# Performance work log

Measured on AMD Instinct MI355X. Metric: run time of the kernel, lower is better.

## Reference

```python
import jax, jax.numpy as jnp
from jax import lax
import numpy as np

B = 8
NUM_ANCHORS = 1047552
PROPOSAL_COUNT = 1000
NMS_THRESHOLD = 0.7
RPN_BBOX_STD_DEV = np.array([0.1, 0.1, 0.2, 0.2], dtype=np.float32)
RPN_NMS_LIMIT = 6000


def setup_inputs() -> dict:
    key = jax.random.key(0)
    k1, k2, k3 = jax.random.split(key, 3)
    rpn_scores = jax.random.uniform(k1, (B, NUM_ANCHORS, 2), dtype=jnp.float32)
    rpn_bbox_delta = jax.random.normal(k2, (B, NUM_ANCHORS, 4), dtype=jnp.float32)
    # Build valid normalized anchors (y1,x1,y2,x2) from uniform randoms.
    u = jax.random.uniform(k3, (NUM_ANCHORS, 4), dtype=jnp.float32)
    cy, cx = u[:, 0], u[:, 1]
    h = u[:, 2] * 0.2 + 0.01
    w = u[:, 3] * 0.2 + 0.01
    anchors = jnp.stack([cy - 0.5 * h, cx - 0.5 * w, cy + 0.5 * h, cx + 0.5 * w], axis=-1)
    anchors = jnp.clip(anchors, 0.0, 1.0)
    return {"rpn_scores": rpn_scores, "rpn_bbox_delta": rpn_bbox_delta, "anchors": anchors}


def _apply_box_deltas(boxes, deltas):
    # boxes: [..., (y1,x1,y2,x2)], deltas: [..., (dy,dx,log(dh),log(dw))]
    h = boxes[..., 2] - boxes[..., 0]
    w = boxes[..., 3] - boxes[..., 1]
    cy = boxes[..., 0] + 0.5 * h + deltas[..., 0] * h
    cx = boxes[..., 1] + 0.5 * w + deltas[..., 1] * w
    h = h * jnp.exp(deltas[..., 2])
    w = w * jnp.exp(deltas[..., 3])
    y1 = cy - 0.5 * h
    x1 = cx - 0.5 * w
    return jnp.stack([y1, x1, y1 + h, x1 + w], axis=-1)


def _nms_indices(boxes):
    # Greedy NMS over boxes already sorted by descending score. boxes: [N,4].
    N = boxes.shape[0]
    areas = (boxes[:, 2] - boxes[:, 0]) * (boxes[:, 3] - boxes[:, 1])

    def body(i, state):
        valid, sel = state
        idx = jnp.argmax(valid)          # first still-valid box = highest score
        has = valid[idx]
        sel = sel.at[i].set(jnp.where(has, idx, -1))
        b = boxes[idx]
        yy1 = jnp.maximum(b[0], boxes[:, 0])
        xx1 = jnp.maximum(b[1], boxes[:, 1])
        yy2 = jnp.minimum(b[2], boxes[:, 2])
        xx2 = jnp.minimum(b[3], boxes[:, 3])
        inter = jnp.maximum(yy2 - yy1, 0.0) * jnp.maximum(xx2 - xx1, 0.0)
        union = areas[idx] + areas - inter
        iou = jnp.where(union > 0, inter / union, 0.0)
        keep = valid & (iou <= NMS_THRESHOLD)
        keep = keep.at[idx].set(False)
        valid = jnp.where(has, keep, valid)
        return valid, sel

    valid0 = jnp.ones((N,), dtype=bool)
    sel0 = jnp.full((PROPOSAL_COUNT,), -1, dtype=jnp.int32)
    _, sel = lax.fori_loop(0, PROPOSAL_COUNT, body, (valid0, sel0))
    return sel


def _nms_single(boxes):
    # boxes: [pre_nms_limit, 4] sorted by score desc -> [proposal_count, 4], zero-padded
    sel = _nms_indices(lax.stop_gradient(boxes))
    props = boxes[jnp.clip(sel, 0)]
    return jnp.where(sel[:, None] >= 0, props, 0.0)


def _forward(rpn_scores, rpn_bbox_delta, anchors):
    scores = rpn_scores[:, :, 1]                                   # [B, A]
    deltas = rpn_bbox_delta * jnp.asarray(RPN_BBOX_STD_DEV)        # [B, A, 4]
    pre_nms_limit = min(RPN_NMS_LIMIT, anchors.shape[0])
    top_scores, ix = lax.top_k(scores, pre_nms_limit)              # [B, pre]
    tgt_deltas = jnp.take_along_axis(deltas, ix[..., None], axis=1)  # [B, pre, 4]
    tgt_anchors = anchors[ix]                                      # [B, pre, 4]
    boxes = _apply_box_deltas(tgt_anchors, tgt_deltas)
    boxes = jnp.clip(boxes, 0.0, 1.0)                              # window (0,0,1,1)
    proposals = jax.vmap(_nms_single)(boxes)                       # [B, proposal_count, 4]
    return proposals


def reference(rpn_scores, rpn_bbox_delta, anchors):
    return _forward(rpn_scores, rpn_bbox_delta, anchors)
```

## Files before the change

kernel.cpp:

```cpp
#include <hip/hip_runtime.h>
#include <stdint.h>

#define NBATCH   8
#define NA       1047552
#define PRE_NMS  6000
#define NPROP    1000
#define BINS     2048
#define HB       64
#define GB       128
#define CAND_CAP 8192
#define NMS_THR  0.7f
#define GBUF     1024
#define SCAP     2048
#define PCHUNK   32
#define PCAP     256
#define REJW     188

#define OFF_HIST  ((size_t)0)
#define OFF_BOFF  (OFF_HIST + (size_t)NBATCH*HB*BINS*2)
#define OFF_BCNT  (OFF_BOFF + (size_t)NBATCH*BINS*4)
#define OFF_CTR   (OFF_BCNT + (size_t)NBATCH*BINS*4)
#define CTR_BYTES ((size_t)(32 + NBATCH*PCHUNK*4 + NBATCH*BINS*4))
#define OFF_CAND  (OFF_CTR + 66624)
#define OFF_BOXES (OFF_CAND + (size_t)NBATCH*CAND_CAP*8)
#define OFF_PAIRS (OFF_BOXES + (size_t)NBATCH*PRE_NMS*16)
#define WS_NEEDED (OFF_PAIRS + (size_t)NBATCH*PCHUNK*PCAP*4)

__device__ __forceinline__ unsigned score_bin(float s) {
    int b = (int)(s * (float)BINS);
    if (b < 0) b = 0;
    if (b > BINS - 1) b = BINS - 1;
    return (unsigned)b;
}

__global__ __launch_bounds__(256) void k_hist(const float* __restrict__ scores,
                                              uint16_t* __restrict__ hist) {
    __shared__ uint32_t lh[BINS];
    const int b = blockIdx.y;
    for (int t = threadIdx.x; t < BINS; t += 256) lh[t] = 0;
    __syncthreads();
    const float4* s4 = reinterpret_cast<const float4*>(scores) + (size_t)b * (NA / 2);
    const int n4 = NA / 2;
    const int stride = gridDim.x * 256;
    for (int i = blockIdx.x * 256 + threadIdx.x; i < n4; i += stride) {
        float4 v = s4[i];
        atomicAdd(&lh[score_bin(v.y)], 1u);
        atomicAdd(&lh[score_bin(v.w)], 1u);
    }
    __syncthreads();
    uint16_t* gh = hist + ((size_t)b * HB + blockIdx.x) * BINS;
    for (int t = threadIdx.x; t < BINS; t += 256) gh[t] = (uint16_t)lh[t];
}

__global__ __launch_bounds__(256) void k_thresh(const uint16_t* __restrict__ hist,
                                                uint32_t* __restrict__ boff,
                                                uint32_t* __restrict__ bcnt,
                                                uint32_t* __restrict__ cbin) {
    __shared__ uint32_t hsum[BINS];
    __shared__ uint32_t csum[256];
    __shared__ int sC;
    const int b = blockIdx.x;
    const int t = threadIdx.x;
    if (t == 0) sC = 0;
    const uint16_t* hb = hist + (size_t)b * HB * BINS;
    uint32_t chunk = 0;
    for (int q = 0; q < 8; ++q) {
        int bin = t * 8 + q;
        uint32_t s = 0;
        for (int k = 0; k < HB; ++k) s += hb[(size_t)k * BINS + bin];
        hsum[bin] = s;
        chunk += s;
    }
    csum[t] = chunk;
    __syncthreads();
    if (t == 0) {
        uint32_t suf = 0;
        for (int c = 255; c >= 0; --c) { uint32_t v = csum[c]; csum[c] = suf; suf += v; }
    }
    __syncthreads();
    uint32_t acc = csum[t];
    for (int q = 7; q >= 0; --q) {
        int bin = t * 8 + q;
        uint32_t h = hsum[bin];
        boff[(size_t)b * BINS + bin] = acc;
        bcnt[(size_t)b * BINS + bin] = h;
        if (acc + h >= PRE_NMS) atomicMax(&sC, bin);
        acc += h;
    }
    __syncthreads();
    if (t == 0) cbin[b] = (uint32_t)sC;
}

__global__ __launch_bounds__(256) void k_gather(const float* __restrict__ scores,
                                                const uint32_t* __restrict__ cbin,
                                                const uint32_t* __restrict__ boff,
                                                uint32_t* __restrict__ binpos,
                                                uint64_t* __restrict__ cand) {
    __shared__ uint64_t keybuf[GBUF];
    __shared__ uint16_t binbuf[GBUF];
    __shared__ uint32_t bcnts[BINS];
    __shared__ uint32_t gbase[BINS];
    __shared__ uint32_t nbuf;
    const int b = blockIdx.y;
    const unsigned C = cbin[b];
    for (int t = threadIdx.x; t < BINS; t += 256) bcnts[t] = 0;
    if (threadIdx.x == 0) nbuf = 0;
    __syncthreads();
    const float4* s4 = reinterpret_cast<const float4*>(scores) + (size_t)b * (NA / 2);
    const int n4 = NA / 2;
    const int stride = gridDim.x * 256;
    uint64_t* cb = cand + (size_t)b * CAND_CAP;
    for (int i = blockIdx.x * 256 + threadIdx.x; i < n4; i += stride) {
        float4 v = s4[i];
        float sc[2] = { v.y, v.w };
        #pragma unroll
        for (int h = 0; h < 2; ++h) {
            unsigned bin = score_bin(sc[h]);
            if (bin >= C) {
                unsigned idx = 2u * (unsigned)i + (unsigned)h;
                uint64_t key = ((uint64_t)__float_as_uint(sc[h]) << 32) | (uint32_t)(~idx);
                unsigned p = atomicAdd(&nbuf, 1u);
                if (p < GBUF) {
                    keybuf[p] = key; binbuf[p] = (uint16_t)bin;
                    atomicAdd(&bcnts[bin], 1u);
                } else {
                    unsigned pos = boff[(size_t)b * BINS + bin] +
                                   atomicAdd(&binpos[(size_t)b * BINS + bin], 1u);
                    if (pos < CAND_CAP) cb[pos] = key;
                }
            }
        }
    }
    __syncthreads();
    for (int t = threadIdx.x; t < BINS; t += 256) {
        uint32_t c = bcnts[t];
        if (c) gbase[t] = boff[(size_t)b * BINS + t] +
                          atomicAdd(&binpos[(size_t)b * BINS + t], c);
        bcnts[t] = 0;
    }
    __syncthreads();
    unsigned n = nbuf; if (n > GBUF) n = GBUF;
    for (unsigned p = threadIdx.x; p < n; p += 256) {
        unsigned bn = binbuf[p];
        unsigned pos = gbase[bn] + atomicAdd(&bcnts[bn], 1u);
        if (pos < CAND_CAP) cb[pos] = keybuf[p];
    }
}

__global__ __launch_bounds__(256) void k_binsort(const uint32_t* __restrict__ cbin,
                                                 const uint32_t* __restrict__ boff,
                                                 const uint32_t* __restrict__ bcnt,
                                                 uint64_t* __restrict__ cand) {
    __shared__ uint64_t s[SCAP];
    const int b = blockIdx.y;
    const unsigned bin = cbin[b] + blockIdx.x;
    if (bin >= BINS) return;
    unsigned cnt = bcnt[(size_t)b * BINS + bin];
    if (cnt == 0) return;
    unsigned start = boff[(size_t)b * BINS + bin];
    if (start >= CAND_CAP) return;
    if (start + cnt > CAND_CAP) cnt = CAND_CAP - start;
    if (cnt > SCAP) cnt = SCAP;
    uint64_t* seg = cand + (size_t)b * CAND_CAP + start;
    for (unsigned i = threadIdx.x; i < SCAP; i += 256)
        s[i] = (i < cnt) ? ~seg[i] : ~0ull;
    __syncthreads();
    for (unsigned k = 2; k <= SCAP; k <<= 1) {
        for (unsigned j = k >> 1; j > 0; j >>= 1) {
            for (unsigned i = threadIdx.x; i < SCAP; i += 256) {
                unsigned ixj = i ^ j;
                if (ixj > i) {
                    uint64_t a = s[i], c = s[ixj];
                    bool up = ((i & k) == 0);
                    if ((a > c) == up) { s[i] = c; s[ixj] = a; }
                }
            }
            __syncthreads();
        }
    }
    for (unsigned i = threadIdx.x; i < cnt; i += 256) seg[i] = ~s[i];
}

__global__ __launch_bounds__(256) void k_decode(const uint64_t* __restrict__ cand,
                                                const float* __restrict__ deltas,
                                                const float* __restrict__ anchors,
                                                float4* __restrict__ boxesOut) {
    const int b = blockIdx.y;
    const int r = blockIdx.x * 256 + threadIdx.x;
    if (r >= PRE_NMS) return;
    uint64_t key = cand[(size_t)b * CAND_CAP + r];
    unsigned idx = ~(uint32_t)key;
    float4 o = make_float4(0.f, 0.f, 0.f, 0.f);
    if (idx < NA) {
        float4 a = reinterpret_cast<const float4*>(anchors)[idx];
        float4 d = reinterpret_cast<const float4*>(deltas)[(size_t)b * NA + idx];
        float h = a.z - a.x, w = a.w - a.y;
        float cy = a.x + 0.5f * h + (d.x * 0.1f) * h;
        float cx = a.y + 0.5f * w + (d.y * 0.1f) * w;
        h = h * expf(d.z * 0.2f);
        w = w * expf(d.w * 0.2f);
        float y1 = cy - 0.5f * h, x1 = cx - 0.5f * w;
        float y2 = y1 + h,        x2 = x1 + w;
        o.x = fminf(fmaxf(y1, 0.f), 1.f);
        o.y = fminf(fmaxf(x1, 0.f), 1.f);
        o.z = fminf(fmaxf(y2, 0.f), 1.f);
        o.w = fminf(fmaxf(x2, 0.f), 1.f);
    }
    boxesOut[(size_t)b * PRE_NMS + r] = o;
}

__global__ __launch_bounds__(64) void k_pairs(const float4* __restrict__ boxes,
                                              uint32_t* __restrict__ pcnt,
                                              uint32_t* __restrict__ pairs) {
    const int tj = blockIdx.x, ti = blockIdx.y, b = blockIdx.z;
    if (ti > tj) return;
    __shared__ float4 bi[64];
    __shared__ float  ai[64];
    const int lane = threadIdx.x;
    const float4* bx = boxes + (size_t)b * PRE_NMS;
    int iIdx = ti * 64 + lane;
    float4 vi0 = (iIdx < PRE_NMS) ? bx[iIdx] : make_float4(0.f, 0.f, 0.f, 0.f);
    bi[lane] = vi0;
    ai[lane] = (vi0.z - vi0.x) * (vi0.w - vi0.y);
    int j = tj * 64 + lane;
    float4 vj = (j < PRE_NMS) ? bx[j] : make_float4(0.f, 0.f, 0.f, 0.f);
    float aj = (vj.z - vj.x) * (vj.w - vj.y);
    __syncthreads();
    for (int it = 0; it < 64; ++it) {
        int i = ti * 64 + it;
        if (i < j && j < PRE_NMS) {
            float4 vi = bi[it];
            float yy1 = fmaxf(vj.x, vi.x);
            float xx1 = fmaxf(vj.y, vi.y);
            float yy2 = fminf(vj.z, vi.z);
            float xx2 = fminf(vj.w, vi.w);
            float ih = yy2 - yy1, iw = xx2 - xx1;
            if (ih > 0.f && iw > 0.f) {
                float inter = ih * iw;
                float uni = aj + ai[it] - inter;
                if (uni > 0.f && (inter / uni) > NMS_THR) {
                    unsigned c = ((unsigned)i + (unsigned)j) & (PCHUNK - 1);
                    unsigned pos = atomicAdd(&pcnt[b * PCHUNK + c], 1u);
                    if (pos < PCAP)
                        pairs[((size_t)b * PCHUNK + c) * PCAP + pos] =
                            ((unsigned)j << 13) | (unsigned)i;
                }
            }
        }
    }
}

__global__ __launch_bounds__(256) void k_nms_emit(const uint32_t* __restrict__ pcnt,
                                                  const uint32_t* __restrict__ pairsIn,
                                                  const float4* __restrict__ boxes,
                                                  float4* __restrict__ out) {
    __shared__ uint32_t sp[PCHUNK * PCAP];
    __shared__ uint32_t cpref[PCHUNK + 1];
    __shared__ uint32_t rejA[REJW], rejB[REJW], pre[REJW + 1];
    __shared__ int changed;
    const int b = blockIdx.x;
    const int tid = threadIdx.x;
    if (tid == 0) {
        unsigned s = 0;
        for (int c = 0; c < PCHUNK; ++c) {
            cpref[c] = s;
            unsigned cc = pcnt[b * PCHUNK + c];
            if (cc > PCAP) cc = PCAP;
            s += cc;
        }
        cpref[PCHUNK] = s;
    }
    for (int t = tid; t < REJW; t += 256) rejA[t] = 0;
    __syncthreads();
    const unsigned np = cpref[PCHUNK];
    for (int c = 0; c < PCHUNK; ++c) {
        unsigned cnt = cpref[c + 1] - cpref[c];
        for (unsigned k = tid; k < cnt; k += 256)
            sp[cpref[c] + k] = pairsIn[((size_t)b * PCHUNK + c) * PCAP + k];
    }
    __syncthreads();
    for (int iter = 0; iter < PRE_NMS; ++iter) {
        for (int t = tid; t < REJW; t += 256) rejB[t] = 0;
        if (tid == 0) changed = 0;
        __syncthreads();
        for (unsigned p = tid; p < np; p += 256) {
            unsigned u = sp[p];
            unsigned j = u >> 13, i = u & 8191u;
            if (!((rejA[i >> 5] >> (i & 31)) & 1u))
                atomicOr(&rejB[j >> 5], 1u << (j & 31));
        }
        __syncthreads();
        for (int t = tid; t < REJW; t += 256) {
            if (rejB[t] != rejA[t]) changed = 1;
            rejA[t] = rejB[t];
        }
        __syncthreads();
        if (!changed) break;
    }
    if (tid == 0) {
        unsigned c2 = 0;
        for (int w = 0; w < REJW; ++w) { pre[w] = c2; c2 += __popc(rejA[w]); }
        pre[REJW] = c2;
    }
    __syncthreads();
    const float4* bx = boxes + (size_t)b * PRE_NMS;
    float4* ob = out + (size_t)b * NPROP;
    for (int j = tid; j < PRE_NMS; j += 256) {
        unsigned w = (unsigned)j >> 5, bit = (unsigned)j & 31;
        if ((rejA[w] >> bit) & 1u) continue;
        unsigned rank = (unsigned)j - (pre[w] + __popc(rejA[w] & ((1u << bit) - 1u)));
        if (rank < NPROP) ob[rank] = bx[j];
    }
}

extern "C" void kernel_launch(void* const* d_in, const int* in_sizes, int n_in,
                              void* d_out, int out_size, void* d_ws, size_t ws_size,
                              hipStream_t stream) {
    const float* scores  = (const float*)d_in[0];
    const float* deltas  = (const float*)d_in[1];
    const float* anchors = (const float*)d_in[2];

    if (ws_size < WS_NEEDED) return;

    char* ws = (char*)d_ws;
    uint16_t* hist   = (uint16_t*)(ws + OFF_HIST);
    uint32_t* boff   = (uint32_t*)(ws + OFF_BOFF);
    uint32_t* bcnt   = (uint32_t*)(ws + OFF_BCNT);
    uint32_t* cbin   = (uint32_t*)(ws + OFF_CTR);
    uint32_t* pcnt   = cbin + NBATCH;
    uint32_t* binpos = pcnt + NBATCH * PCHUNK;
    uint64_t* cand   = (uint64_t*)(ws + OFF_CAND);
    float4*   boxes  = (float4*)(ws + OFF_BOXES);
    uint32_t* pairs  = (uint32_t*)(ws + OFF_PAIRS);

    hipMemsetAsync((void*)cbin, 0, CTR_BYTES, stream);
    hipMemsetAsync(d_out, 0, (size_t)NBATCH * NPROP * 4 * sizeof(float), stream);

    k_hist   <<<dim3(HB, NBATCH), 256, 0, stream>>>(scores, hist);
    k_thresh <<<NBATCH, 256, 0, stream>>>(hist, boff, bcnt, cbin);
    k_gather <<<dim3(GB, NBATCH), 256, 0, stream>>>(scores, cbin, boff, binpos, cand);
    k_binsort<<<dim3(128, NBATCH), 256, 0, stream>>>(cbin, boff, bcnt, cand);
    k_decode <<<dim3((PRE_NMS + 255) / 256, NBATCH), 256, 0, stream>>>(cand, deltas, anchors, boxes);
    k_pairs  <<<dim3((PRE_NMS + 63) / 64, (PRE_NMS + 63) / 64, NBATCH), 64, 0, stream>>>(boxes, pcnt, pairs);
    k_nms_emit<<<NBATCH, 256, 0, stream>>>(pcnt, pairs, boxes, (float4*)d_out);
}
```

Before: 481.1 us.

## Retile pairwise IoU kernel, shrink bitonic sort size, vectorize histogram reduction

The pairwise IoU kernel now uses 64x256 tiles with 256-thread blocks in place of 64x64 tiles with 64-thread blocks. It takes a fast branch-free path for off-diagonal tiles, replaces the IoU division with a multiply compare, and pads out-of-range boxes with sentinel coordinates. The per-bin bitonic sort now sorts only the next power of two above the bin count instead of always sorting 2048 entries. The threshold kernel reads the 16-bit histograms as packed 32-bit words. Together these cut launch count, redundant sorting work and memory transactions, at the cost of some wasted work on diagonal tiles.

```diff
diff --git a/kernel.cpp b/kernel.cpp
--- a/kernel.cpp
+++ b/kernel.cpp
@@ -15,6 +15,8 @@
 #define PCHUNK   32
 #define PCAP     256
 #define REJW     188
+#define PTI      64
+#define PTJ      256
 
 #define OFF_HIST  ((size_t)0)
 #define OFF_BOFF  (OFF_HIST + (size_t)NBATCH*HB*BINS*2)
@@ -62,16 +64,24 @@
     const int b = blockIdx.x;
     const int t = threadIdx.x;
     if (t == 0) sC = 0;
-    const uint16_t* hb = hist + (size_t)b * HB * BINS;
-    uint32_t chunk = 0;
-    for (int q = 0; q < 8; ++q) {
-        int bin = t * 8 + q;
-        uint32_t s = 0;
-        for (int k = 0; k < HB; ++k) s += hb[(size_t)k * BINS + bin];
-        hsum[bin] = s;
-        chunk += s;
-    }
-    csum[t] = chunk;
+    const uint32_t* hb32 =
+        reinterpret_cast<const uint32_t*>(hist + (size_t)b * HB * BINS);
+    for (int p = t; p < BINS / 2; p += 256) {
+        uint32_t s0 = 0, s1 = 0;
+        for (int k = 0; k < HB; ++k) {
+            uint32_t v = hb32[(size_t)k * (BINS / 2) + p];
+            s0 += v & 0xffffu;
+            s1 += v >> 16;
+        }
+        hsum[2 * p]     = s0;
+        hsum[2 * p + 1] = s1;
+    }
+    __syncthreads();
+    {
+        uint32_t c = 0;
+        for (int q = 0; q < 8; ++q) c += hsum[t * 8 + q];
+        csum[t] = c;
+    }
     __syncthreads();
     if (t == 0) {
         uint32_t suf = 0;
@@ -161,13 +171,15 @@
     if (start >= CAND_CAP) return;
     if (start + cnt > CAND_CAP) cnt = CAND_CAP - start;
     if (cnt > SCAP) cnt = SCAP;
+    unsigned m = 256;
+    while (m < cnt) m <<= 1;
     uint64_t* seg = cand + (size_t)b * CAND_CAP + start;
-    for (unsigned i = threadIdx.x; i < SCAP; i += 256)
+    for (unsigned i = threadIdx.x; i < m; i += 256)
         s[i] = (i < cnt) ? ~seg[i] : ~0ull;
     __syncthreads();
-    for (unsigned k = 2; k <= SCAP; k <<= 1) {
+    for (unsigned k = 2; k <= m; k <<= 1) {
         for (unsigned j = k >> 1; j > 0; j >>= 1) {
-            for (unsigned i = threadIdx.x; i < SCAP; i += 256) {
+            for (unsigned i = threadIdx.x; i < m; i += 256) {
                 unsigned ixj = i ^ j;
                 if (ixj > i) {
                     uint64_t a = s[i], c = s[ixj];
@@ -209,42 +221,66 @@
     boxesOut[(size_t)b * PRE_NMS + r] = o;
 }
 
-__global__ __launch_bounds__(64) void k_pairs(const float4* __restrict__ boxes,
-                                              uint32_t* __restrict__ pcnt,
-                                              uint32_t* __restrict__ pairs) {
-    const int tj = blockIdx.x, ti = blockIdx.y, b = blockIdx.z;
-    if (ti > tj) return;
-    __shared__ float4 bi[64];
-    __shared__ float  ai[64];
-    const int lane = threadIdx.x;
+__global__ __launch_bounds__(256) void k_pairs(const float4* __restrict__ boxes,
+                                               uint32_t* __restrict__ pcnt,
+                                               uint32_t* __restrict__ pairs) {
+    const int jb = blockIdx.x;
+    const int ib = blockIdx.y;
+    const int b  = blockIdx.z;
+    const int i0 = ib * PTI;
+    const int j0 = jb * PTJ;
+    if (i0 > j0 + PTJ - 1) return;
+    __shared__ float4 bi[PTI];
+    __shared__ float  ai[PTI];
+    const int tid = threadIdx.x;
     const float4* bx = boxes + (size_t)b * PRE_NMS;
-    int iIdx = ti * 64 + lane;
-    float4 vi0 = (iIdx < PRE_NMS) ? bx[iIdx] : make_float4(0.f, 0.f, 0.f, 0.f);
-    bi[lane] = vi0;
-    ai[lane] = (vi0.z - vi0.x) * (vi0.w - vi0.y);
-    int j = tj * 64 + lane;
-    float4 vj = (j < PRE_NMS) ? bx[j] : make_float4(0.f, 0.f, 0.f, 0.f);
-    float aj = (vj.z - vj.x) * (vj.w - vj.y);
-    __syncthreads();
-    for (int it = 0; it < 64; ++it) {
-        int i = ti * 64 + it;
-        if (i < j && j < PRE_NMS) {
+    if (tid < PTI) {
+        int ii = i0 + tid;
+        float4 v = (ii < PRE_NMS) ? bx[ii] : make_float4(2.f, 2.f, 2.f, 2.f);
+        bi[tid] = v;
+        ai[tid] = (v.z - v.x) * (v.w - v.y);
+    }
+    const int j = j0 + tid;
+    float4 vj = (j < PRE_NMS) ? bx[j] : make_float4(2.f, 2.f, 2.f, 2.f);
+    const float aj = (vj.z - vj.x) * (vj.w - vj.y);
+    __syncthreads();
+    uint32_t* pc = pcnt + b * PCHUNK;
+    uint32_t* pb = pairs + (size_t)b * PCHUNK * PCAP;
+    const bool touchesDiag = (i0 + PTI - 1 >= j0);
+    if (touchesDiag) {
+        for (int it = 0; it < PTI; ++it) {
+            int i = i0 + it;
+            if (i >= j) continue;
             float4 vi = bi[it];
             float yy1 = fmaxf(vj.x, vi.x);
             float xx1 = fmaxf(vj.y, vi.y);
             float yy2 = fminf(vj.z, vi.z);
             float xx2 = fminf(vj.w, vi.w);
             float ih = yy2 - yy1, iw = xx2 - xx1;
-            if (ih > 0.f && iw > 0.f) {
-                float inter = ih * iw;
-                float uni = aj + ai[it] - inter;
-                if (uni > 0.f && (inter / uni) > NMS_THR) {
-                    unsigned c = ((unsigned)i + (unsigned)j) & (PCHUNK - 1);
-                    unsigned pos = atomicAdd(&pcnt[b * PCHUNK + c], 1u);
-                    if (pos < PCAP)
-                        pairs[((size_t)b * PCHUNK + c) * PCAP + pos] =
-                            ((unsigned)j << 13) | (unsigned)i;
-                }
+            float inter = ih * iw;
+            float uni = aj + ai[it] - inter;
+            if (ih > 0.f && iw > 0.f && inter > NMS_THR * uni) {
+                unsigned c = ((unsigned)i + (unsigned)j) & (PCHUNK - 1);
+                unsigned pos = atomicAdd(&pc[c], 1u);
+                if (pos < PCAP) pb[(size_t)c * PCAP + pos] = ((unsigned)j << 13) | (unsigned)i;
+            }
+        }
+    } else {
+        #pragma unroll 4
+        for (int it = 0; it < PTI; ++it) {
+            float4 vi = bi[it];
+            float yy1 = fmaxf(vj.x, vi.x);
+            float xx1 = fmaxf(vj.y, vi.y);
+            float yy2 = fminf(vj.z, vi.z);
+            float xx2 = fminf(vj.w, vi.w);
+            float ih = yy2 - yy1, iw = xx2 - xx1;
+            float inter = ih * iw;
+            float uni = aj + ai[it] - inter;
+            if (ih > 0.f && iw > 0.f && inter > NMS_THR * uni) {
+                unsigned i = (unsigned)(i0 + it);
+                unsigned c = (i + (unsigned)j) & (PCHUNK - 1);
+                unsigned pos = atomicAdd(&pc[c], 1u);
+                if (pos < PCAP) pb[(size_t)c * PCAP + pos] = ((unsigned)j << 13) | i;
             }
         }
     }
@@ -341,6 +377,7 @@
     k_gather <<<dim3(GB, NBATCH), 256, 0, stream>>>(scores, cbin, boff, binpos, cand);
     k_binsort<<<dim3(128, NBATCH), 256, 0, stream>>>(cbin, boff, bcnt, cand);
     k_decode <<<dim3((PRE_NMS + 255) / 256, NBATCH), 256, 0, stream>>>(cand, deltas, anchors, boxes);
-    k_pairs  <<<dim3((PRE_NMS + 63) / 64, (PRE_NMS + 63) / 64, NBATCH), 64, 0, stream>>>(boxes, pcnt, pairs);
+    k_pairs  <<<dim3((PRE_NMS + PTJ - 1) / PTJ, (PRE_NMS + PTI - 1) / PTI, NBATCH),
+               256, 0, stream>>>(boxes, pcnt, pairs);
     k_nms_emit<<<NBATCH, 256, 0, stream>>>(pcnt, pairs, boxes, (float4*)d_out);
 }
```

New measurement: 431.5 us. -10.3%, faster.
